# Kernel optimization log

Measured on AMD Instinct MI355X. Metric: run time of the kernel, lower is better.

## Reference

```python
import jax, jax.numpy as jnp
import numpy as np

T, D, O, L, R = 8192, 4096, 4096, 8, 16  # tokens, in_dim, out_dim, max_loras, lora_rank


def setup_inputs() -> dict:
    key = jax.random.key(0)
    k0, k1, k2, k3, k4 = jax.random.split(key, 5)
    x = jax.random.normal(k0, (T, D), dtype=jnp.float32)
    weight = jax.random.normal(k1, (O, D), dtype=jnp.float32) * 0.02   # base Linear weight
    lora_a = jax.random.normal(k2, (L, R, D), dtype=jnp.float32) * 0.02  # stacked A (slice dim squeezed)
    lora_b = jax.random.normal(k3, (L, O, R), dtype=jnp.float32) * 0.02  # stacked B
    token_lora_idx = jax.random.randint(k4, (T,), 0, L, dtype=jnp.int32)  # per-token adapter id
    return {"x": x, "weight": weight, "lora_a": lora_a, "lora_b": lora_b,
            "token_lora_idx": token_lora_idx}


def reference(x, weight, lora_a, lora_b, token_lora_idx):
    # base linear (no bias)
    base = jnp.einsum('td,od->to', x, weight)
    # punica add_lora_linear, single slice, scale = 1.0:
    # per-token gather of A/B expressed as a one-hot contraction (small L, rank R)
    onehot = jax.nn.one_hot(token_lora_idx, lora_a.shape[0], dtype=x.dtype)  # [T, L]
    shrink = jnp.einsum('td,lrd->tlr', x, lora_a)          # [T, L, R] (tiny: R=16)
    s = jnp.einsum('tlr,tl->tr', shrink, onehot)           # select this token's adapter
    delta = jnp.einsum('tr,lor,tl->to', s, lora_b, onehot) # expand + scatter-add
    return base + delta
```

## Files before the change

kernel.cpp:

```cpp
#include <hip/hip_runtime.h>
#include <hip/hip_bf16.h>
#include <stdint.h>

#define T_TOK 8192
#define DIM 4096
#define ODIM 4096
#define NL 8
#define RANK 16
#define KAUG 4224
#define NKT (KAUG / 64)

__device__ __forceinline__ uint16_t f2b(float x) {
    uint32_t u = __builtin_bit_cast(uint32_t, x);
    u += 0x7fffu + ((u >> 16) & 1u);
    return (uint16_t)(u >> 16);
}

typedef __attribute__((ext_vector_type(4))) float floatx4;
typedef __attribute__((ext_vector_type(8))) __bf16 bf16x8;

__device__ __forceinline__ void load_lds16(const uint16_t* g, uint16_t* l) {
    __builtin_amdgcn_global_load_lds(
        (const __attribute__((address_space(1))) uint32_t*)g,
        (__attribute__((address_space(3))) uint32_t*)l, 16, 0, 0);
}

__global__ __launch_bounds__(256) void pack_all(const float* __restrict__ x,
                                                const float* __restrict__ W,
                                                const float* __restrict__ la,
                                                const float* __restrict__ lb,
                                                uint16_t* __restrict__ xaug,
                                                uint16_t* __restrict__ waug,
                                                uint16_t* __restrict__ aall) {
    int b = blockIdx.x;
    int tid = threadIdx.x;
    const float* src;
    uint16_t* dst;
    if (b < ODIM)               { src = W  + (size_t)b * DIM;                 dst = waug + (size_t)b * KAUG; }
    else if (b < ODIM + T_TOK)  { int t = b - ODIM;
                                  src = x  + (size_t)t * DIM;                 dst = xaug + (size_t)t * KAUG; }
    else                        { int r = b - ODIM - T_TOK;
                                  src = la + (size_t)r * DIM;                 dst = aall + (size_t)r * DIM; }
#pragma unroll
    for (int k = 0; k < 4; ++k) {
        int i4 = k * 256 + tid;
        float4 v = ((const float4*)src)[i4];
        ushort4 bv;
        bv.x = f2b(v.x); bv.y = f2b(v.y); bv.z = f2b(v.z); bv.w = f2b(v.w);
        *(ushort4*)(dst + (size_t)i4 * 4) = bv;
    }
    if (b < ODIM && tid < NL * RANK) {
        int l = tid >> 4, r = tid & 15;
        dst[DIM + tid] = f2b(lb[((size_t)l * ODIM + b) * RANK + r]);
    }
}

#define SBM 32
__global__ __launch_bounds__(256) void shrink_gemm(const uint16_t* __restrict__ xa,
                                                   const uint16_t* __restrict__ aall,
                                                   const int* __restrict__ idx,
                                                   uint16_t* __restrict__ xaug) {
    __shared__ uint16_t sA[SBM * 64];
    __shared__ uint16_t sB[128 * 64];
    int tid = threadIdx.x, lane = tid & 63, wid = tid >> 6;
    int bm = blockIdx.x;
    int q = lane >> 4, r16 = lane & 15;

    int rS = tid >> 3;
    int kcS = (tid & 7) ^ (rS & 7);
    const uint16_t* gA = xa + (size_t)(bm * SBM + rS) * KAUG + kcS * 8;
    const uint16_t* gB0 = aall + (size_t)(rS) * DIM + kcS * 8;
    const uint16_t* gB1 = aall + (size_t)(32 + rS) * DIM + kcS * 8;
    const uint16_t* gB2 = aall + (size_t)(64 + rS) * DIM + kcS * 8;
    const uint16_t* gB3 = aall + (size_t)(96 + rS) * DIM + kcS * 8;
    uint16_t* lA  = sA + wid * 512;
    uint16_t* lB0 = sB + wid * 512;
    uint16_t* lB1 = sB + 2048 + wid * 512;
    uint16_t* lB2 = sB + 4096 + wid * 512;
    uint16_t* lB3 = sB + 6144 + wid * 512;

    int sw0 = (q ^ (r16 & 7)) * 8;
    int sw1 = ((4 + q) ^ (r16 & 7)) * 8;

    floatx4 acc[2][2];
#pragma unroll
    for (int i = 0; i < 2; ++i)
#pragma unroll
        for (int j = 0; j < 2; ++j) acc[i][j] = (floatx4){0.f, 0.f, 0.f, 0.f};

    for (int k0 = 0; k0 < DIM; k0 += 64) {
        __syncthreads();
        load_lds16(gA + k0, lA);
        load_lds16(gB0 + k0, lB0);
        load_lds16(gB1 + k0, lB1);
        load_lds16(gB2 + k0, lB2);
        load_lds16(gB3 + k0, lB3);
        __syncthreads();
#pragma unroll
        for (int kk = 0; kk < 2; ++kk) {
            int sw = kk ? sw1 : sw0;
            bf16x8 af[2], bv[2];
#pragma unroll
            for (int i = 0; i < 2; ++i)
                af[i] = *(const bf16x8*)(sA + (i * 16 + r16) * 64 + sw);
#pragma unroll
            for (int j = 0; j < 2; ++j)
                bv[j] = *(const bf16x8*)(sB + (wid * 32 + j * 16 + r16) * 64 + sw);
#pragma unroll
            for (int i = 0; i < 2; ++i)
#pragma unroll
                for (int j = 0; j < 2; ++j)
                    acc[i][j] = __builtin_amdgcn_mfma_f32_16x16x32_bf16(af[i], bv[j], acc[i][j], 0, 0, 0);
        }
    }
#pragma unroll
    for (int i = 0; i < 2; ++i) {
#pragma unroll
        for (int j = 0; j < 2; ++j) {
            int p = wid * 32 + j * 16 + r16;
            int lp = p >> 4;
#pragma unroll
            for (int e = 0; e < 4; ++e) {
                int t = bm * SBM + i * 16 + q * 4 + e;
                uint16_t v = (idx[t] == lp) ? f2b(acc[i][j][e]) : (uint16_t)0;
                xaug[(size_t)t * KAUG + DIM + p] = v;
            }
        }
    }
}

#define GBM 256
#define GBN 256

__global__ __launch_bounds__(512) void gemm_aug8(const uint16_t* __restrict__ A,
                                                 const uint16_t* __restrict__ B,
                                                 float* __restrict__ C) {
    __shared__ uint16_t sA[2][GBM * 64];
    __shared__ uint16_t sB[2][GBN * 64];

    int tid = threadIdx.x;
    int lane = tid & 63, wid = tid >> 6;
    int q = lane >> 4, r16 = lane & 15;
    int wm = (wid >> 2) * 128;
    int wn = (wid & 3) * 64;

    int cpx = gridDim.x >> 3;
    int wgid = (blockIdx.x & 7) * cpx + (blockIdx.x >> 3);
    int bn = wgid & 15;
    int bm = wgid >> 4;

    int rS = tid >> 3;
    int cS = (tid & 7) ^ (rS & 7);
    const uint16_t* gA0 = A + (size_t)(bm * GBM + rS) * KAUG + cS * 8;
    const uint16_t* gB0 = B + (size_t)(bn * GBN + rS) * KAUG + cS * 8;
    int ldsOff = wid * 512;

    auto stageA2 = [&](int bufi, int part, int tk) {
        const uint16_t* g = gA0 + (size_t)tk * 64;
        uint16_t* l = &sA[bufi][ldsOff];
        load_lds16(g + (size_t)(part * 64) * KAUG,       l + part * 4096);
        load_lds16(g + (size_t)((part + 2) * 64) * KAUG, l + (part + 2) * 4096);
    };
    auto stageBh = [&](int bufi, int half, int tk) {
        const uint16_t* g = gB0 + (size_t)(half * 128) * KAUG + (size_t)tk * 64;
        uint16_t* l = &sB[bufi][half * 8192 + ldsOff];
        load_lds16(g, l);
        load_lds16(g + (size_t)64 * KAUG, l + 4096);
    };

    int swz[2] = { ((0 + q) ^ (r16 & 7)) * 8, ((4 + q) ^ (r16 & 7)) * 8 };

    bf16x8 aH[4][2];
    bf16x8 bfv[4][2];
    floatx4 acc[8][4];
#pragma unroll
    for (int i = 0; i < 8; ++i)
#pragma unroll
        for (int j = 0; j < 4; ++j) acc[i][j] = (floatx4){0.f, 0.f, 0.f, 0.f};

    auto rdA = [&](int b, int mh) {
#pragma unroll
        for (int mf = 0; mf < 4; ++mf)
#pragma unroll
            for (int kk = 0; kk < 2; ++kk)
                aH[mf][kk] = *(const bf16x8*)&sA[b][(wm + mh * 64 + mf * 16 + r16) * 64 + swz[kk]];
    };
    auto rdBq = [&](int b, int nh) {
#pragma unroll
        for (int nf = 0; nf < 2; ++nf)
#pragma unroll
            for (int kk = 0; kk < 2; ++kk)
                bfv[nh * 2 + nf][kk] = *(const bf16x8*)&sB[b][(wn + (nh * 2 + nf) * 16 + r16) * 64 + swz[kk]];
    };
    auto mmaQ = [&](int mh, int nh) {
        __builtin_amdgcn_s_setprio(1);
#pragma unroll
        for (int mf = 0; mf < 4; ++mf)
#pragma unroll
            for (int nf = 0; nf < 2; ++nf)
#pragma unroll
                for (int kk = 0; kk < 2; ++kk)
                    acc[mh * 4 + mf][nh * 2 + nf] = __builtin_amdgcn_mfma_f32_16x16x32_bf16(
                        aH[mf][kk], bfv[nh * 2 + nf][kk], acc[mh * 4 + mf][nh * 2 + nf], 0, 0, 0);
        __builtin_amdgcn_s_setprio(0);
    };

#define BAR  __builtin_amdgcn_s_barrier()
#define VM6  asm volatile("s_waitcnt vmcnt(6)" ::: "memory")
#define VM8  asm volatile("s_waitcnt vmcnt(8)" ::: "memory")
#define VM0  asm volatile("s_waitcnt vmcnt(0)" ::: "memory")

    stageA2(0, 0, 0); stageBh(0, 0, 0); stageBh(0, 1, 0); stageA2(0, 1, 0);
    stageA2(1, 0, 1); stageBh(1, 0, 1);

#pragma unroll 1
    for (int i = 0; i < NKT / 2; ++i) {
        int t1 = 2 * i + 1, t2 = 2 * i + 2, t3 = 2 * i + 3;
        bool full = (t2 < NKT);

        VM6; BAR;
        rdA(0, 0); rdBq(0, 0);
        stageBh(1, 1, t1);
        mmaQ(0, 0);
        BAR;
        rdBq(0, 1);
        stageA2(1, 1, t1);
        mmaQ(0, 1);
        VM8; BAR;
        rdA(0, 1);
        if (full) stageA2(0, 0, t2);
        mmaQ(1, 0);
        BAR;
        if (full) stageBh(0, 0, t2);
        mmaQ(1, 1);

        if (full) { VM6; } else { VM0; }
        BAR;
        rdA(1, 0); rdBq(1, 0);
        if (full) stageBh(0, 1, t2);
        mmaQ(0, 0);
        BAR;
        rdBq(1, 1);
        if (full) stageA2(0, 1, t2);
        mmaQ(0, 1);
        if (full) { VM8; } else { VM0; }
        BAR;
        rdA(1, 1);
        if (t3 < NKT) stageA2(1, 0, t3);
        mmaQ(1, 0);
        BAR;
        if (t3 < NKT) stageBh(1, 0, t3);
        mmaQ(1, 1);
    }

#pragma unroll
    for (int mf = 0; mf < 8; ++mf) {
#pragma unroll
        for (int nf = 0; nf < 4; ++nf) {
            int col = bn * GBN + wn + nf * 16 + r16;
            int rowb = bm * GBM + wm + mf * 16 + q * 4;
#pragma unroll
            for (int e = 0; e < 4; ++e)
                C[(size_t)(rowb + e) * ODIM + col] = acc[mf][nf][e];
        }
    }
#undef BAR
#undef VM6
#undef VM8
#undef VM0
}

extern "C" void kernel_launch(void* const* d_in, const int* in_sizes, int n_in,
                              void* d_out, int out_size, void* d_ws, size_t ws_size,
                              hipStream_t stream) {
    const float* x  = (const float*)d_in[0];
    const float* W  = (const float*)d_in[1];
    const float* la = (const float*)d_in[2];
    const float* lb = (const float*)d_in[3];
    const int* idx  = (const int*)d_in[4];
    float* out = (float*)d_out;

    uint16_t* xaug = (uint16_t*)d_ws;
    uint16_t* waug = xaug + (size_t)T_TOK * KAUG;
    uint16_t* aall = waug + (size_t)ODIM * KAUG;

    hipLaunchKernelGGL(pack_all, dim3(ODIM + T_TOK + NL * RANK), dim3(256), 0, stream,
                       x, W, la, lb, xaug, waug, aall);
    hipLaunchKernelGGL(shrink_gemm, dim3(T_TOK / SBM), dim3(256), 0, stream,
                       xaug, aall, idx, xaug);
    hipLaunchKernelGGL(gemm_aug8, dim3((T_TOK / GBM) * (ODIM / GBN)), dim3(512), 0, stream,
                       xaug, waug, out);
}
```

Measured before the change: 551.3 us.

## Software-pipeline LDS fragment reads ahead of MFMA quadrants in GEMM loop

The main K loop is rescheduled so each LDS fragment read for the next quadrant is issued right after the current quadrant's MFMAs, before the following barrier, and the first read is hoisted into a prologue. Explicit lgkmcnt(0) waits and sched_barriers pin the ordering, and the vmcnt thresholds are retuned for the new placement of global-to-LDS loads. The goal is to hide LDS read latency behind MFMA work and tighten the overlap of global loads. It depends on subtle wait counts, so a miscount could cause stale LDS reads or extra stalls.

```diff
diff --git a/kernel.cpp b/kernel.cpp
--- a/kernel.cpp
+++ b/kernel.cpp
@@ -206,51 +206,64 @@
     };
 
 #define BAR  __builtin_amdgcn_s_barrier()
+#define SB0  __builtin_amdgcn_sched_barrier(0)
+#define LGK0 { asm volatile("s_waitcnt lgkmcnt(0)" ::: "memory"); SB0; }
+#define VM0  asm volatile("s_waitcnt vmcnt(0)" ::: "memory")
+#define VM1  asm volatile("s_waitcnt vmcnt(1)" ::: "memory")
+#define VM2  asm volatile("s_waitcnt vmcnt(2)" ::: "memory")
+#define VM3  asm volatile("s_waitcnt vmcnt(3)" ::: "memory")
 #define VM6  asm volatile("s_waitcnt vmcnt(6)" ::: "memory")
-#define VM8  asm volatile("s_waitcnt vmcnt(8)" ::: "memory")
-#define VM0  asm volatile("s_waitcnt vmcnt(0)" ::: "memory")
 
     stageA2(0, 0, 0); stageBh(0, 0, 0); stageBh(0, 1, 0); stageA2(0, 1, 0);
     stageA2(1, 0, 1); stageBh(1, 0, 1);
+    VM6;
+    BAR;
+    rdA(0, 0); rdBq(0, 0); SB0;
 
 #pragma unroll 1
     for (int i = 0; i < NKT / 2; ++i) {
         int t1 = 2 * i + 1, t2 = 2 * i + 2, t3 = 2 * i + 3;
         bool full = (t2 < NKT);
 
-        VM6; BAR;
-        rdA(0, 0); rdBq(0, 0);
+        BAR;
         stageBh(1, 1, t1);
+        LGK0;
         mmaQ(0, 0);
-        BAR;
-        rdBq(0, 1);
+        rdBq(0, 1); SB0;
+        VM3; BAR;
         stageA2(1, 1, t1);
+        LGK0;
         mmaQ(0, 1);
-        VM8; BAR;
-        rdA(0, 1);
+        rdA(0, 1); SB0;
+        BAR;
         if (full) stageA2(0, 0, t2);
+        LGK0;
         mmaQ(1, 0);
+        if (full) { VM2; } else { VM1; }
         BAR;
         if (full) stageBh(0, 0, t2);
         mmaQ(1, 1);
-
-        if (full) { VM6; } else { VM0; }
-        BAR;
-        rdA(1, 0); rdBq(1, 0);
+        rdA(1, 0); rdBq(1, 0); SB0;
+        BAR;
         if (full) stageBh(0, 1, t2);
+        LGK0;
         mmaQ(0, 0);
-        BAR;
-        rdBq(1, 1);
+        rdBq(1, 1); SB0;
+        if (full) { VM3; } else { VM0; }
+        BAR;
         if (full) stageA2(0, 1, t2);
+        LGK0;
         mmaQ(0, 1);
-        if (full) { VM8; } else { VM0; }
-        BAR;
-        rdA(1, 1);
+        rdA(1, 1); SB0;
+        BAR;
         if (t3 < NKT) stageA2(1, 0, t3);
+        LGK0;
         mmaQ(1, 0);
+        if (full) { VM2; }
         BAR;
         if (t3 < NKT) stageBh(1, 0, t3);
         mmaQ(1, 1);
+        if (full) { rdA(0, 0); rdBq(0, 0); SB0; }
     }
 
 #pragma unroll
@@ -265,9 +278,13 @@
         }
     }
 #undef BAR
+#undef SB0
+#undef LGK0
+#undef VM0
+#undef VM1
+#undef VM2
+#undef VM3
 #undef VM6
-#undef VM8
-#undef VM0
 }
 
 extern "C" void kernel_launch(void* const* d_in, const int* in_sizes, int n_in,
```

Result: no change. 557.0 us (+1.0%).
